# Kernel tuning notes

Measured on AMD Instinct MI355X. Metric: run time of the kernel, lower is better.

The kernel has to match this reference:

```python
import jax, jax.numpy as jnp
import numpy as np

WAY = 5
EPS = 1e-12  # torch F.normalize eps


def setup_inputs() -> dict:
    key = jax.random.key(0)
    k1, k2, k3, k4 = jax.random.split(key, 4)
    n_support, n_queries = 25, 200
    f_g, f_l, d = 16, 64, 512
    return {
        "support_set_global": jax.random.normal(k1, (n_support, f_g, d), jnp.float32),
        "support_set_local": jax.random.normal(k2, (n_support, f_l, d), jnp.float32),
        "support_labels": (jnp.arange(n_support) % WAY).astype(jnp.int64),
        "queries_global": jax.random.normal(k3, (n_queries, f_g, d), jnp.float32),
        "queries_local": jax.random.normal(k4, (n_queries, f_l, d), jnp.float32),
    }


def _l2norm(x):
    # torch F.normalize(dim=1) with eps clamp
    n = jnp.linalg.norm(x, axis=-1, keepdims=True)
    return x / jnp.maximum(n, EPS)


def reference(support_set_global, support_set_local, support_labels,
              queries_global, queries_local):
    # Dropout is identity in eval mode; omitted for a deterministic reference.
    S = jnp.concatenate([support_set_global, support_set_local], axis=1)  # [nS, F, D]
    Q = jnp.concatenate([queries_global, queries_local], axis=1)          # [nQ, F, D]
    nS, F, D = S.shape
    nQ = Q.shape[0]

    Sn = _l2norm(S.reshape(nS * F, D))
    Qn = _l2norm(Q.reshape(nQ * F, D))

    # cosine-sim matmul: [nS*F, nQ*F]
    sim = Sn @ Qn.T
    # view(nS, F, nQ, F).transpose(2,1) -> [nS, nQ, F, F]
    sim = sim.reshape(nS, F, nQ, F).transpose(0, 2, 1, 3)
    dmat = 1.0 - sim

    # squared Frobenius norm over last two dims, keepdim -> [nS, nQ, 1, 1]
    fro2 = jnp.sum(dmat * dmat, axis=(-2, -1))  # [nS, nQ]
    # dists.min(3)[0].sum(2) + dists.min(2)[0].sum(2) over singleton dims == 2 * fro2
    cum_dists = 2.0 * fro2  # [nS, nQ]

    # per-class mean over support rows (class-wise gather-mean)
    counts = jax.ops.segment_sum(jnp.ones((nS,), cum_dists.dtype), support_labels,
                                 num_segments=WAY)                       # [WAY]
    class_sum = jax.ops.segment_sum(cum_dists, support_labels, num_segments=WAY)  # [WAY, nQ]
    class_dists = class_sum / counts[:, None]

    logits = -class_dists.T  # [nQ, WAY]
    return logits
```

## Files before the change

kernel.cpp:

```cpp
#include <hip/hip_runtime.h>

#define NS 25
#define NQ 200
#define FG 16
#define FL 64
#define FTOT 80
#define D 512
#define WAY 5
#define MROWS 2000
#define MPAD 2080
#define NROWS 16000

typedef unsigned char u8;
typedef __attribute__((ext_vector_type(4))) float floatx4;
typedef __attribute__((ext_vector_type(4))) int intx4;

__device__ inline void gload_lds16(const void* g, void* l) {
    __builtin_amdgcn_global_load_lds(
        (const __attribute__((address_space(1))) unsigned int*)g,
        (__attribute__((address_space(3))) unsigned int*)l, 16, 0, 0);
}

__global__ void normalize_kernel(const float* __restrict__ sg, const float* __restrict__ sl,
                                 const float* __restrict__ qg, const float* __restrict__ ql,
                                 u8* __restrict__ Sn, u8* __restrict__ Qn,
                                 const int* __restrict__ labels,
                                 float* __restrict__ out, float* __restrict__ rcnt) {
    if (blockIdx.x == 4500) {
        intx4 z = {0, 0, 0, 0};
        intx4* pad = (intx4*)(Sn + (size_t)MROWS * D);
        for (int i = threadIdx.x; i < (MPAD - MROWS) * D / 16; i += 256) pad[i] = z;
        for (int i = threadIdx.x; i < NQ * WAY; i += 256) out[i] = 0.f;
        if (threadIdx.x == 0) {
            int counts[WAY] = {0, 0, 0, 0, 0};
            for (int s = 0; s < NS; ++s) counts[labels[s]]++;
            for (int c = 0; c < WAY; ++c) rcnt[c] = 1.0f / (float)(counts[c] ? counts[c] : 1);
        }
        return;
    }
    int wave = (blockIdx.x * blockDim.x + threadIdx.x) >> 6;
    int lane = threadIdx.x & 63;
    const int totalRows = MROWS + NROWS;
    if (wave >= totalRows) return;

    const float* src;
    u8* dst;
    if (wave < MROWS) {
        int s = wave / FTOT, f = wave % FTOT;
        src = (f < FG) ? sg + (size_t)(s * FG + f) * D
                       : sl + (size_t)(s * FL + (f - FG)) * D;
        dst = Sn + (size_t)wave * D;
    } else {
        int r = wave - MROWS;
        int q = r / FTOT, f = r % FTOT;
        src = (f < FG) ? qg + (size_t)(q * FG + f) * D
                       : ql + (size_t)(q * FL + (f - FG)) * D;
        dst = Qn + (size_t)r * D;
    }

    float4 v0 = ((const float4*)src)[2 * lane];
    float4 v1 = ((const float4*)src)[2 * lane + 1];
    float ss = v0.x*v0.x + v0.y*v0.y + v0.z*v0.z + v0.w*v0.w
             + v1.x*v1.x + v1.y*v1.y + v1.z*v1.z + v1.w*v1.w;
    #pragma unroll
    for (int off = 32; off > 0; off >>= 1) ss += __shfl_xor(ss, off, 64);
    float scale = 1.0f / fmaxf(sqrtf(ss), 1e-12f);

    int w0 = __builtin_amdgcn_cvt_pk_fp8_f32(v0.x * scale, v0.y * scale, 0, false);
    w0     = __builtin_amdgcn_cvt_pk_fp8_f32(v0.z * scale, v0.w * scale, w0, true);
    int w1 = __builtin_amdgcn_cvt_pk_fp8_f32(v1.x * scale, v1.y * scale, 0, false);
    w1     = __builtin_amdgcn_cvt_pk_fp8_f32(v1.z * scale, v1.w * scale, w1, true);
    ((int2*)dst)[lane] = make_int2(w0, w1);
}

__global__ __launch_bounds__(256, 3) void gemm_kernel(const u8* __restrict__ Sn,
                                                      const u8* __restrict__ Qn,
                                                      const int* __restrict__ labels,
                                                      const float* __restrict__ rcnt,
                                                      float* __restrict__ out) {
    __shared__ u8 As[160][128];
    __shared__ u8 Bs[160][128];

    const int bx = blockIdx.x;
    const int by = blockIdx.y;
    const int tid = threadIdx.x;
    const int lane = tid & 63;
    const int w = tid >> 6;
    const int lm = lane & 15;
    const int lq = lane >> 4;
    const int wr = w >> 1;
    const int wc = w & 1;

    floatx4 acc[5][5];
    #pragma unroll
    for (int i = 0; i < 5; ++i)
        #pragma unroll
        for (int j = 0; j < 5; ++j) acc[i][j] = (floatx4){0.f, 0.f, 0.f, 0.f};

    const u8* Sbase = Sn + (size_t)by * 160 * D;
    const u8* Qbase = Qn + (size_t)bx * 160 * D;

    const u8* gsrc = (w < 2) ? Sbase : Qbase;
    u8* ldst = (w < 2) ? (u8*)As : (u8*)Bs;
    const int sl0 = (w & 1) * 10;
    const int grow = lane >> 3;
    const int gc = lane & 7;

    #pragma unroll 1
    for (int kc = 0; kc < 4; ++kc) {
        const int k0 = kc * 128;
        __syncthreads();
        #pragma unroll
        for (int t = 0; t < 10; ++t) {
            const int sl = sl0 + t;
            const int r = sl * 8 + grow;
            const int cp = gc ^ ((r >> 1) & 7);
            gload_lds16(gsrc + (size_t)r * D + k0 + cp * 16, ldst + sl * 1024);
        }
        __syncthreads();
        #pragma unroll
        for (int ks = 0; ks < 4; ++ks) {
            long long a[5], b[5];
            #pragma unroll
            for (int i = 0; i < 5; ++i) {
                const int r = wr * 80 + i * 16 + lm;
                const int c = (ks * 2 + (lq >> 1)) ^ ((r >> 1) & 7);
                a[i] = *(const long long*)(&As[r][c * 16 + (lq & 1) * 8]);
            }
            #pragma unroll
            for (int j = 0; j < 5; ++j) {
                const int r = wc * 80 + j * 16 + lm;
                const int c = (ks * 2 + (lq >> 1)) ^ ((r >> 1) & 7);
                b[j] = *(const long long*)(&Bs[r][c * 16 + (lq & 1) * 8]);
            }
            #pragma unroll
            for (int i = 0; i < 5; ++i)
                #pragma unroll
                for (int j = 0; j < 5; ++j)
                    acc[i][j] = __builtin_amdgcn_mfma_f32_16x16x32_fp8_fp8(a[i], b[j], acc[i][j], 0, 0, 0);
        }
    }

    float local = 0.f;
    #pragma unroll
    for (int i = 0; i < 5; ++i)
        #pragma unroll
        for (int j = 0; j < 5; ++j)
            #pragma unroll
            for (int r = 0; r < 4; ++r) {
                const float d = 1.0f - acc[i][j][r];
                local = fmaf(d, d, local);
            }
    #pragma unroll
    for (int off = 32; off > 0; off >>= 1) local += __shfl_down(local, off, 64);

    const int sIdx = by * 2 + wr;
    const int qIdx = bx * 2 + wc;
    if (lane == 0 && sIdx < NS) {
        const int c = labels[sIdx];
        atomicAdd(&out[qIdx * WAY + c], -2.0f * local * rcnt[c]);
    }
}

extern "C" void kernel_launch(void* const* d_in, const int* in_sizes, int n_in,
                              void* d_out, int out_size, void* d_ws, size_t ws_size,
                              hipStream_t stream) {
    const float* sg = (const float*)d_in[0];
    const float* sl = (const float*)d_in[1];
    const int* labels = (const int*)d_in[2];
    const float* qg = (const float*)d_in[3];
    const float* ql = (const float*)d_in[4];
    float* out = (float*)d_out;

    u8* Sn = (u8*)d_ws;
    u8* Qn = Sn + (size_t)MPAD * D;
    float* rcnt = (float*)(Qn + (size_t)NROWS * D);

    normalize_kernel<<<4501, 256, 0, stream>>>(sg, sl, qg, ql, Sn, Qn, labels, out, rcnt);
    dim3 g2(100, 13);
    gemm_kernel<<<g2, 256, 0, stream>>>(Sn, Qn, labels, rcnt, out);
}
```

Before: 111.6 us.

## Switch to 16x16x128 scaled FP8 MFMA with 128-bit LDS fragment loads

Replaces the four K-steps of 16x16x32 fp8 MFMAs per 128-wide chunk with a single gfx950 mfma_scale 16x16x128 f8f6f4 instruction per tile, using unit scales (0x7F exponent). Fragments are now loaded as two 16-byte LDS reads per lane with precomputed swizzled offsets instead of 8-byte reads. This cuts MFMA issue count and LDS instruction count, and the loop is restructured so B fragments are loaded per column. The K ordering across lanes changes to match the new instruction's layout, which is valid only if the A and B fragments are permuted the same way.

```diff
diff --git a/kernel.cpp b/kernel.cpp
--- a/kernel.cpp
+++ b/kernel.cpp
@@ -14,6 +14,7 @@
 typedef unsigned char u8;
 typedef __attribute__((ext_vector_type(4))) float floatx4;
 typedef __attribute__((ext_vector_type(4))) int intx4;
+typedef __attribute__((ext_vector_type(8))) int intx8;
 
 __device__ inline void gload_lds16(const void* g, void* l) {
     __builtin_amdgcn_global_load_lds(
@@ -78,8 +79,8 @@
                                                       const int* __restrict__ labels,
                                                       const float* __restrict__ rcnt,
                                                       float* __restrict__ out) {
-    __shared__ u8 As[160][128];
-    __shared__ u8 Bs[160][128];
+    __shared__ __align__(16) u8 As[160][128];
+    __shared__ __align__(16) u8 Bs[160][128];
 
     const int bx = blockIdx.x;
     const int by = blockIdx.y;
@@ -106,6 +107,17 @@
     const int grow = lane >> 3;
     const int gc = lane & 7;
 
+    union frag { intx8 v; intx4 h[2]; };
+
+    int aoff[5], boff[5];
+    #pragma unroll
+    for (int i = 0; i < 5; ++i) {
+        const int ra = wr * 80 + i * 16 + lm;
+        aoff[i] = ra * 128 + (((2 * lq) ^ ((ra >> 1) & 7)) * 16);
+        const int rb = wc * 80 + i * 16 + lm;
+        boff[i] = rb * 128 + (((2 * lq) ^ ((rb >> 1) & 7)) * 16);
+    }
+
     #pragma unroll 1
     for (int kc = 0; kc < 4; ++kc) {
         const int k0 = kc * 128;
@@ -118,26 +130,23 @@
             gload_lds16(gsrc + (size_t)r * D + k0 + cp * 16, ldst + sl * 1024);
         }
         __syncthreads();
+
+        frag af[5];
         #pragma unroll
-        for (int ks = 0; ks < 4; ++ks) {
-            long long a[5], b[5];
-            #pragma unroll
-            for (int i = 0; i < 5; ++i) {
-                const int r = wr * 80 + i * 16 + lm;
-                const int c = (ks * 2 + (lq >> 1)) ^ ((r >> 1) & 7);
-                a[i] = *(const long long*)(&As[r][c * 16 + (lq & 1) * 8]);
-            }
-            #pragma unroll
-            for (int j = 0; j < 5; ++j) {
-                const int r = wc * 80 + j * 16 + lm;
-                const int c = (ks * 2 + (lq >> 1)) ^ ((r >> 1) & 7);
-                b[j] = *(const long long*)(&Bs[r][c * 16 + (lq & 1) * 8]);
-            }
+        for (int i = 0; i < 5; ++i) {
+            af[i].h[0] = *(const intx4*)((const u8*)As + aoff[i]);
+            af[i].h[1] = *(const intx4*)((const u8*)As + (aoff[i] ^ 16));
+        }
+        #pragma unroll
+        for (int j = 0; j < 5; ++j) {
+            frag bf;
+            bf.h[0] = *(const intx4*)((const u8*)Bs + boff[j]);
+            bf.h[1] = *(const intx4*)((const u8*)Bs + (boff[j] ^ 16));
             #pragma unroll
             for (int i = 0; i < 5; ++i)
-                #pragma unroll
-                for (int j = 0; j < 5; ++j)
-                    acc[i][j] = __builtin_amdgcn_mfma_f32_16x16x32_fp8_fp8(a[i], b[j], acc[i][j], 0, 0, 0);
+                acc[i][j] = __builtin_amdgcn_mfma_scale_f32_16x16x128_f8f6f4(
+                    af[i].v, bf.v, acc[i][j], 0, 0,
+                    0, 0x7F7F7F7F, 0, 0x7F7F7F7F);
         }
     }
 
```

Result: slower. 134.8 us (+20.8%).
